# Kernel optimization log

Measured on AMD Instinct MI355X. Metric: run time of the kernel, lower is better.

Reference implementation:

```python
import jax, jax.numpy as jnp
import numpy as np
from jax import lax

B, T, D = 4096, 2048, 10
H = 4          # num_units
OUT = 30       # output_dim


def setup_inputs() -> dict:
    key = jax.random.key(0)
    ks = jax.random.split(key, 7)
    s_ih = 1.0 / np.sqrt(H)
    return {
        "X": jax.random.normal(ks[0], (B, T, D), dtype=jnp.float32),
        # PyTorch LSTM params, gate order (i, f, g, o)
        "W_ih": jax.random.uniform(ks[1], (4 * H, D), minval=-s_ih, maxval=s_ih, dtype=jnp.float32),
        "W_hh": jax.random.uniform(ks[2], (4 * H, H), minval=-s_ih, maxval=s_ih, dtype=jnp.float32),
        "b_ih": jax.random.uniform(ks[3], (4 * H,), minval=-s_ih, maxval=s_ih, dtype=jnp.float32),
        "b_hh": jax.random.uniform(ks[4], (4 * H,), minval=-s_ih, maxval=s_ih, dtype=jnp.float32),
        "W_out": jax.random.uniform(ks[5], (OUT, H), minval=-s_ih, maxval=s_ih, dtype=jnp.float32),
        "b_out": jax.random.uniform(ks[6], (OUT,), minval=-s_ih, maxval=s_ih, dtype=jnp.float32),
    }


def _lstm_last_hidden(X, W_ih, W_hh, b_ih, b_hh):
    # Precompute input projections for all timesteps: [B, T, 4H]
    x_proj = jnp.einsum('btd,gd->btg', X, W_ih) + b_ih + b_hh
    h0 = jnp.zeros((X.shape[0], W_hh.shape[1]), dtype=X.dtype)
    c0 = jnp.zeros_like(h0)

    def step(carry, xt):  # xt: [B, 4H]
        h, c = carry
        gates = xt + h @ W_hh.T
        i, f, g, o = jnp.split(gates, 4, axis=-1)
        i = jax.nn.sigmoid(i)
        f = jax.nn.sigmoid(f)
        g = jnp.tanh(g)
        o = jax.nn.sigmoid(o)
        c = f * c + i * g
        h = o * jnp.tanh(c)
        return (h, c), None

    (h_T, _), _ = lax.scan(step, (h0, c0), jnp.swapaxes(x_proj, 0, 1))
    return h_T  # [B, H]


def reference(X, W_ih, W_hh, b_ih, b_hh, W_out, b_out):
    h_T = _lstm_last_hidden(X, W_ih, W_hh, b_ih, b_hh)
    # dropout p=0 is a no-op; softmax over output_dim
    logits = h_T @ W_out.T + b_out
    return jax.nn.softmax(logits, axis=-1)
```

## Files before the change

kernel.cpp:

```cpp
#include <hip/hip_runtime.h>
#include <stdint.h>

#define B_TOT 4096
#define T_LEN 2048
#define D_IN  10
#define OUT_N 30
#define TT    64
#define NT    (T_LEN/TT)
#define SMP_BLK 16
#define TILE_FLOATS (TT*SMP_BLK*D_IN)
#define NLD   (TILE_FLOATS/(4*64))

#define GLD4(gptr, lptr) __builtin_amdgcn_global_load_lds( \
    (const __attribute__((address_space(1))) void*)(gptr),  \
    (__attribute__((address_space(3))) void*)(lptr), 4, 0, 0)

template<int CTRL>
__device__ __forceinline__ float dppf(float x) {
    return __int_as_float(
        __builtin_amdgcn_mov_dpp(__float_as_int(x), CTRL, 0xF, 0xF, true));
}

__device__ __forceinline__ float fast_exp2(float x) {
#if __has_builtin(__builtin_amdgcn_exp2f)
    return __builtin_amdgcn_exp2f(x);
#else
    float r; asm("v_exp_f32 %0, %1" : "=v"(r) : "v"(x)); return r;
#endif
}

__launch_bounds__(256, 1)
__global__ void lstm_scan_kernel(const float* __restrict__ X,
                                 const float* __restrict__ W_ih,
                                 const float* __restrict__ W_hh,
                                 const float* __restrict__ b_ih,
                                 const float* __restrict__ b_hh,
                                 float* __restrict__ hT)
{
    __shared__ float lds[2][TILE_FLOATS];

    const int tid  = threadIdx.x;
    const int lane = tid & 63;
    const int g    = tid >> 4;
    const int u    = (tid >> 2) & 3;
    const int tau  = tid & 3;
    const int r    = tau * 4 + u;
    const int w    = tid >> 6;

    const float KT = -2.8853900817779268f;
    const float KS = -1.4426950408889634f;
    const float mneg = (tau == 2) ? KT : KS;
    const float k1   = (tau == 0) ? KT : ((tau == 1) ? 1.0f : 2.0f);
    const float k0   = (tau == 2) ? -1.0f : 0.0f;

    float wih[10];
    #pragma unroll
    for (int d0 = 0; d0 < 10; ++d0) wih[d0] = W_ih[r*10 + d0] * mneg;
    const float whhA = W_hh[r*4 +  u        ] * mneg;
    const float whhB = W_hh[r*4 + ((u+3)&3)] * mneg;
    const float whhC = W_hh[r*4 + ((u+2)&3)] * mneg;
    const float whhD = W_hh[r*4 + ((u+1)&3)] * mneg;
    const float bsum = (b_ih[r] + b_hh[r]) * mneg;

    uint32_t voff[NLD];
    const uint32_t samp0 = (uint32_t)blockIdx.x * SMP_BLK;
    #pragma unroll
    for (int kk = 0; kk < NLD; ++kk) {
        int p   = (w*NLD + kk)*64 + lane;
        int t   = p / 160;
        int rem = p - t*160;
        int s   = rem / 10;
        int d0  = rem - s*10;
        voff[kk] = (samp0 + (uint32_t)s) * (uint32_t)(T_LEN*D_IN*4)
                 + (uint32_t)(t*40 + d0*4);
    }
    const char* Xc = (const char*)X;

    #pragma unroll
    for (int kk = 0; kk < NLD; ++kk)
        GLD4(Xc + voff[kk], &lds[0][(w*NLD+kk)*64]);
    __syncthreads();

    float cs = 0.f, hown = 0.f;

    for (int tile = 0; tile < NT; ++tile) {
        const int cur = tile & 1;
        if (tile + 1 < NT) {
            const uint32_t add = (uint32_t)(tile+1) * (uint32_t)(TT*D_IN*4);
            #pragma unroll
            for (int kk = 0; kk < NLD; ++kk)
                GLD4(Xc + (voff[kk] + add), &lds[cur^1][(w*NLD+kk)*64]);
        }
        const float2* xp = (const float2*)((const char*)&lds[cur][0] + g*40);

        float2 xB[5];
        #pragma unroll
        for (int k = 0; k < 5; ++k) xB[k] = xp[80 + k];
        float xaccA;
        {
            float2 x0 = xp[0], x1 = xp[1], x2 = xp[2], x3 = xp[3], x4 = xp[4];
            float acc = bsum;
            acc = fmaf(wih[0], x0.x, acc); acc = fmaf(wih[1], x0.y, acc);
            acc = fmaf(wih[2], x1.x, acc); acc = fmaf(wih[3], x1.y, acc);
            acc = fmaf(wih[4], x2.x, acc); acc = fmaf(wih[5], x2.y, acc);
            acc = fmaf(wih[6], x3.x, acc); acc = fmaf(wih[7], x3.y, acc);
            acc = fmaf(wih[8], x4.x, acc); acc = fmaf(wih[9], x4.y, acc);
            xaccA = acc;
        }

        #pragma unroll
        for (int t = 0; t < TT; ++t) {
            float2 xN[5];
            if (t + 2 < TT) {
                #pragma unroll
                for (int k = 0; k < 5; ++k) xN[k] = xp[(t+2)*80 + k];
            }
            float xaccB = 0.f;
            if (t + 1 < TT) {
                float acc = bsum;
                acc = fmaf(wih[0], xB[0].x, acc); acc = fmaf(wih[1], xB[0].y, acc);
                acc = fmaf(wih[2], xB[1].x, acc); acc = fmaf(wih[3], xB[1].y, acc);
                acc = fmaf(wih[4], xB[2].x, acc); acc = fmaf(wih[5], xB[2].y, acc);
                acc = fmaf(wih[6], xB[3].x, acc); acc = fmaf(wih[7], xB[3].y, acc);
                acc = fmaf(wih[8], xB[4].x, acc); acc = fmaf(wih[9], xB[4].y, acc);
                xaccB = acc;
            }
            float hB = dppf<0x124>(hown);
            float hC = dppf<0x128>(hown);
            float hD = dppf<0x12C>(hown);
            float u1 = fmaf(whhA, hown, xaccA);
            float acc = fmaf(whhB, hB, u1) + fmaf(whhD, hD, whhC * hC);
            float e  = fast_exp2(acc);
            float a  = fmaf(k1, __builtin_amdgcn_rcpf(1.0f + e), k0);
            float gi = dppf<0x00>(a);
            float gf = dppf<0x55>(a);
            float gg = dppf<0xAA>(a);
            float go = dppf<0xFF>(a);
            float mgo = -0.5f * go;
            cs = fmaf(gf, cs, gi * gg);
            float e2 = fast_exp2(cs);
            float r2 = __builtin_amdgcn_rcpf(1.0f + e2);
            hown = fmaf(go, r2, mgo);
            #pragma unroll
            for (int k = 0; k < 5; ++k) xB[k] = xN[k];
            xaccA = xaccB;
        }
        __syncthreads();
    }

    if (tau == 0) hT[(samp0 + g)*4 + u] = hown;
}

__global__ void head_kernel(const float* __restrict__ hT,
                            const float* __restrict__ W_out,
                            const float* __restrict__ b_out,
                            float* __restrict__ out)
{
    int b = blockIdx.x * blockDim.x + threadIdx.x;
    if (b >= B_TOT) return;
    float4 h = ((const float4*)hT)[b];
    float lg[OUT_N];
    float m = -1e30f;
    #pragma unroll
    for (int o = 0; o < OUT_N; ++o) {
        float v = b_out[o];
        v = fmaf(W_out[o*4+0], h.x, v);
        v = fmaf(W_out[o*4+1], h.y, v);
        v = fmaf(W_out[o*4+2], h.z, v);
        v = fmaf(W_out[o*4+3], h.w, v);
        lg[o] = v;
        m = fmaxf(m, v);
    }
    float s = 0.f;
    #pragma unroll
    for (int o = 0; o < OUT_N; ++o) {
        float e = fast_exp2((lg[o] - m) * 1.4426950408889634f);
        lg[o] = e;
        s += e;
    }
    float rs = 1.0f / s;
    #pragma unroll
    for (int o = 0; o < OUT_N; ++o) out[(size_t)b*OUT_N + o] = lg[o] * rs;
}

extern "C" void kernel_launch(void* const* d_in, const int* in_sizes, int n_in,
                              void* d_out, int out_size, void* d_ws, size_t ws_size,
                              hipStream_t stream)
{
    const float* X     = (const float*)d_in[0];
    const float* W_ih  = (const float*)d_in[1];
    const float* W_hh  = (const float*)d_in[2];
    const float* b_ih  = (const float*)d_in[3];
    const float* b_hh  = (const float*)d_in[4];
    const float* W_out = (const float*)d_in[5];
    const float* b_out = (const float*)d_in[6];
    float* out = (float*)d_out;
    float* hTs = (float*)d_ws;

    lstm_scan_kernel<<<B_TOT/SMP_BLK, 256, 0, stream>>>(X, W_ih, W_hh, b_ih, b_hh, hTs);
    head_kernel<<<B_TOT/256, 256, 0, stream>>>(hTs, W_out, b_out, out);
}
```

Baseline: 247.1 us.

## Split LSTM scan into producer and consumer warps with LDS handoff

Each block now has 512 threads. Four producer waves load X chunks into LDS and compute the input projections into a double-buffered LDS gate buffer. Four consumer waves run only the serial recurrence, reading the precomputed projections. The goal is to take the input-projection FMAs and the X-tile loads off the latency-critical recurrent chain. The trade-off is extra LDS traffic, a barrier every 32 steps, and a higher thread count per block with launch bounds of two blocks per CU.

```diff
diff --git a/kernel.cpp b/kernel.cpp
--- a/kernel.cpp
+++ b/kernel.cpp
@@ -5,11 +5,13 @@
 #define T_LEN 2048
 #define D_IN  10
 #define OUT_N 30
-#define TT    64
-#define NT    (T_LEN/TT)
+#define CSTEP 32
+#define NCH   (T_LEN/CSTEP)
 #define SMP_BLK 16
-#define TILE_FLOATS (TT*SMP_BLK*D_IN)
-#define NLD   (TILE_FLOATS/(4*64))
+#define XBUF_F (CSTEP*SMP_BLK*D_IN)
+#define ABUF_F (CSTEP*SMP_BLK*16)
+#define NLD   (XBUF_F/(4*64))
+#define CH_BYTES (CSTEP*D_IN*4)
 
 #define GLD4(gptr, lptr) __builtin_amdgcn_global_load_lds( \
     (const __attribute__((address_space(1))) void*)(gptr),  \
@@ -29,7 +31,7 @@
 #endif
 }
 
-__launch_bounds__(256, 1)
+__launch_bounds__(512, 2)
 __global__ void lstm_scan_kernel(const float* __restrict__ X,
                                  const float* __restrict__ W_ih,
                                  const float* __restrict__ W_hh,
@@ -37,118 +39,127 @@
                                  const float* __restrict__ b_hh,
                                  float* __restrict__ hT)
 {
-    __shared__ float lds[2][TILE_FLOATS];
+    __shared__ float xbuf[2][XBUF_F];
+    __shared__ float abuf[2][ABUF_F];
 
     const int tid  = threadIdx.x;
     const int lane = tid & 63;
-    const int g    = tid >> 4;
-    const int u    = (tid >> 2) & 3;
-    const int tau  = tid & 3;
-    const int r    = tau * 4 + u;
     const int w    = tid >> 6;
+    const int lr   = lane & 15;
+    const int grp  = lane >> 4;
+    const int u    = (lr >> 2) & 3;
+    const int tau  = lr & 3;
+    const int rw   = tau * 4 + u;
+    const uint32_t samp0 = (uint32_t)blockIdx.x * SMP_BLK;
 
     const float KT = -2.8853900817779268f;
     const float KS = -1.4426950408889634f;
     const float mneg = (tau == 2) ? KT : KS;
-    const float k1   = (tau == 0) ? KT : ((tau == 1) ? 1.0f : 2.0f);
-    const float k0   = (tau == 2) ? -1.0f : 0.0f;
-
-    float wih[10];
-    #pragma unroll
-    for (int d0 = 0; d0 < 10; ++d0) wih[d0] = W_ih[r*10 + d0] * mneg;
-    const float whhA = W_hh[r*4 +  u        ] * mneg;
-    const float whhB = W_hh[r*4 + ((u+3)&3)] * mneg;
-    const float whhC = W_hh[r*4 + ((u+2)&3)] * mneg;
-    const float whhD = W_hh[r*4 + ((u+1)&3)] * mneg;
-    const float bsum = (b_ih[r] + b_hh[r]) * mneg;
-
-    uint32_t voff[NLD];
-    const uint32_t samp0 = (uint32_t)blockIdx.x * SMP_BLK;
-    #pragma unroll
-    for (int kk = 0; kk < NLD; ++kk) {
-        int p   = (w*NLD + kk)*64 + lane;
-        int t   = p / 160;
-        int rem = p - t*160;
-        int s   = rem / 10;
-        int d0  = rem - s*10;
-        voff[kk] = (samp0 + (uint32_t)s) * (uint32_t)(T_LEN*D_IN*4)
-                 + (uint32_t)(t*40 + d0*4);
+
+    if (w >= 4) {
+        const int pw = w - 4;
+        const int sg = pw * 4 + grp;
+        float wih[10];
+        #pragma unroll
+        for (int d0 = 0; d0 < 10; ++d0) wih[d0] = W_ih[rw*10 + d0] * mneg;
+        const float bsum = (b_ih[rw] + b_hh[rw]) * mneg;
+
+        uint32_t voff[NLD];
+        #pragma unroll
+        for (int kk = 0; kk < NLD; ++kk) {
+            int p   = (pw*NLD + kk)*64 + lane;
+            int t   = p / 160;
+            int rem = p - t*160;
+            int s   = rem / 10;
+            int d0  = rem - s*10;
+            voff[kk] = (samp0 + (uint32_t)s) * (uint32_t)(T_LEN*D_IN*4)
+                     + (uint32_t)(t*40 + d0*4);
+        }
+        const char* Xc = (const char*)X;
+
+        auto produce = [&](int bb) {
+            #pragma unroll 4
+            for (int t = 0; t < CSTEP; ++t) {
+                const float2* xp =
+                    (const float2*)&xbuf[bb][(t*SMP_BLK + sg)*10];
+                float2 x0 = xp[0], x1 = xp[1], x2 = xp[2],
+                       x3 = xp[3], x4 = xp[4];
+                float acc = bsum;
+                acc = fmaf(wih[0], x0.x, acc); acc = fmaf(wih[1], x0.y, acc);
+                acc = fmaf(wih[2], x1.x, acc); acc = fmaf(wih[3], x1.y, acc);
+                acc = fmaf(wih[4], x2.x, acc); acc = fmaf(wih[5], x2.y, acc);
+                acc = fmaf(wih[6], x3.x, acc); acc = fmaf(wih[7], x3.y, acc);
+                acc = fmaf(wih[8], x4.x, acc); acc = fmaf(wih[9], x4.y, acc);
+                abuf[bb][(t*SMP_BLK + sg)*16 + lr] = acc;
+            }
+        };
+
+        #pragma unroll
+        for (int kk = 0; kk < NLD; ++kk)
+            GLD4(Xc + voff[kk], &xbuf[0][(pw*NLD+kk)*64]);
+        __syncthreads();
+        #pragma unroll
+        for (int kk = 0; kk < NLD; ++kk)
+            GLD4(Xc + (voff[kk] + CH_BYTES), &xbuf[1][(pw*NLD+kk)*64]);
+        produce(0);
+        __syncthreads();
+
+        for (int k = 0; k < NCH; ++k) {
+            if (k + 1 < NCH) {
+                if (k + 2 < NCH) {
+                    const uint32_t add = (uint32_t)(k+2) * CH_BYTES;
+                    #pragma unroll
+                    for (int kk = 0; kk < NLD; ++kk)
+                        GLD4(Xc + (voff[kk] + add),
+                             &xbuf[k&1][(pw*NLD+kk)*64]);
+                }
+                produce((k+1)&1);
+            }
+            __syncthreads();
+        }
+    } else {
+        const int sg = w * 4 + grp;
+        const float k1 = (tau == 0) ? KT : ((tau == 1) ? 1.0f : 2.0f);
+        const float k0 = (tau == 2) ? -1.0f : 0.0f;
+        const float whhA = W_hh[rw*4 +  u        ] * mneg;
+        const float whhB = W_hh[rw*4 + ((u+3)&3)] * mneg;
+        const float whhC = W_hh[rw*4 + ((u+2)&3)] * mneg;
+        const float whhD = W_hh[rw*4 + ((u+1)&3)] * mneg;
+
+        __syncthreads();
+        __syncthreads();
+
+        float cs = 0.f, hown = 0.f;
+        for (int k = 0; k < NCH; ++k) {
+            const float* ab = &abuf[k&1][sg*16 + lr];
+            float xr0 = ab[0];
+            float xr1 = ab[256];
+            #pragma unroll
+            for (int t = 0; t < CSTEP; ++t) {
+                float xr2 = 0.f;
+                if (t + 2 < CSTEP) xr2 = ab[(t+2)*256];
+                float hB = dppf<0x124>(hown);
+                float hC = dppf<0x128>(hown);
+                float hD = dppf<0x12C>(hown);
+                float u1 = fmaf(whhA, hown, xr0);
+                float acc = fmaf(whhB, hB, u1) + fmaf(whhD, hD, whhC * hC);
+                float e  = fast_exp2(acc);
+                float a  = fmaf(k1, __builtin_amdgcn_rcpf(1.0f + e), k0);
+                float gi = dppf<0x00>(a);
+                float gf = dppf<0x55>(a);
+                float gg = dppf<0xAA>(a);
+                float go = dppf<0xFF>(a);
+                float mgo = -0.5f * go;
+                cs = fmaf(gf, cs, gi * gg);
+                float e2 = fast_exp2(cs);
+                float r2 = __builtin_amdgcn_rcpf(1.0f + e2);
+                hown = fmaf(go, r2, mgo);
+                xr0 = xr1; xr1 = xr2;
+            }
+            __syncthreads();
+        }
+        if (tau == 0) hT[(samp0 + sg)*4 + u] = hown;
     }
-    const char* Xc = (const char*)X;
-
-    #pragma unroll
-    for (int kk = 0; kk < NLD; ++kk)
-        GLD4(Xc + voff[kk], &lds[0][(w*NLD+kk)*64]);
-    __syncthreads();
-
-    float cs = 0.f, hown = 0.f;
-
-    for (int tile = 0; tile < NT; ++tile) {
-        const int cur = tile & 1;
-        if (tile + 1 < NT) {
-            const uint32_t add = (uint32_t)(tile+1) * (uint32_t)(TT*D_IN*4);
-            #pragma unroll
-            for (int kk = 0; kk < NLD; ++kk)
-                GLD4(Xc + (voff[kk] + add), &lds[cur^1][(w*NLD+kk)*64]);
-        }
-        const float2* xp = (const float2*)((const char*)&lds[cur][0] + g*40);
-
-        float2 xB[5];
-        #pragma unroll
-        for (int k = 0; k < 5; ++k) xB[k] = xp[80 + k];
-        float xaccA;
-        {
-            float2 x0 = xp[0], x1 = xp[1], x2 = xp[2], x3 = xp[3], x4 = xp[4];
-            float acc = bsum;
-            acc = fmaf(wih[0], x0.x, acc); acc = fmaf(wih[1], x0.y, acc);
-            acc = fmaf(wih[2], x1.x, acc); acc = fmaf(wih[3], x1.y, acc);
-            acc = fmaf(wih[4], x2.x, acc); acc = fmaf(wih[5], x2.y, acc);
-            acc = fmaf(wih[6], x3.x, acc); acc = fmaf(wih[7], x3.y, acc);
-            acc = fmaf(wih[8], x4.x, acc); acc = fmaf(wih[9], x4.y, acc);
-            xaccA = acc;
-        }
-
-        #pragma unroll
-        for (int t = 0; t < TT; ++t) {
-            float2 xN[5];
-            if (t + 2 < TT) {
-                #pragma unroll
-                for (int k = 0; k < 5; ++k) xN[k] = xp[(t+2)*80 + k];
-            }
-            float xaccB = 0.f;
-            if (t + 1 < TT) {
-                float acc = bsum;
-                acc = fmaf(wih[0], xB[0].x, acc); acc = fmaf(wih[1], xB[0].y, acc);
-                acc = fmaf(wih[2], xB[1].x, acc); acc = fmaf(wih[3], xB[1].y, acc);
-                acc = fmaf(wih[4], xB[2].x, acc); acc = fmaf(wih[5], xB[2].y, acc);
-                acc = fmaf(wih[6], xB[3].x, acc); acc = fmaf(wih[7], xB[3].y, acc);
-                acc = fmaf(wih[8], xB[4].x, acc); acc = fmaf(wih[9], xB[4].y, acc);
-                xaccB = acc;
-            }
-            float hB = dppf<0x124>(hown);
-            float hC = dppf<0x128>(hown);
-            float hD = dppf<0x12C>(hown);
-            float u1 = fmaf(whhA, hown, xaccA);
-            float acc = fmaf(whhB, hB, u1) + fmaf(whhD, hD, whhC * hC);
-            float e  = fast_exp2(acc);
-            float a  = fmaf(k1, __builtin_amdgcn_rcpf(1.0f + e), k0);
-            float gi = dppf<0x00>(a);
-            float gf = dppf<0x55>(a);
-            float gg = dppf<0xAA>(a);
-            float go = dppf<0xFF>(a);
-            float mgo = -0.5f * go;
-            cs = fmaf(gf, cs, gi * gg);
-            float e2 = fast_exp2(cs);
-            float r2 = __builtin_amdgcn_rcpf(1.0f + e2);
-            hown = fmaf(go, r2, mgo);
-            #pragma unroll
-            for (int k = 0; k < 5; ++k) xB[k] = xN[k];
-            xaccA = xaccB;
-        }
-        __syncthreads();
-    }
-
-    if (tau == 0) hT[(samp0 + g)*4 + u] = hown;
 }
 
 __global__ void head_kernel(const float* __restrict__ hT,
@@ -197,6 +208,6 @@
     float* out = (float*)d_out;
     float* hTs = (float*)d_ws;
 
-    lstm_scan_kernel<<<B_TOT/SMP_BLK, 256, 0, stream>>>(X, W_ih, W_hh, b_ih, b_hh, hTs);
+    lstm_scan_kernel<<<B_TOT/SMP_BLK, 512, 0, stream>>>(X, W_ih, W_hh, b_ih, b_hh, hTs);
     head_kernel<<<B_TOT/256, 256, 0, stream>>>(hTs, W_out, b_out, out);
 }
```

Result: slower. 252.2 us (+2.1%).
